# Kernel optimization log

Hardware: AMD Instinct MI355X
Metric: run time of the kernel (lower is better)

The kernel has to match this reference:

```python
import jax, jax.numpy as jnp
import numpy as np

N = 100000       # num nodes
E = 3200000      # num edges (avg degree 32)
F_IN = 128       # num_node_features
HID = 16         # hidden dim hard-coded in Net
C = 10           # num_classes


def setup_inputs() -> dict:
    key = jax.random.key(0)
    k1, k2, k3, k4 = jax.random.split(key, 4)
    x = jax.random.normal(k1, (N, F_IN), dtype=jnp.float32)
    edge_index = jax.random.randint(k2, (2, E), 0, N, dtype=jnp.int32)
    W1 = jax.random.normal(k3, (F_IN, HID), dtype=jnp.float32) * 0.05
    b1 = jnp.zeros((HID,), dtype=jnp.float32)
    W2 = jax.random.normal(k4, (HID, C), dtype=jnp.float32) * 0.05
    b2 = jnp.zeros((C,), dtype=jnp.float32)
    return {"x": x, "edge_index": edge_index, "W1": W1, "b1": b1, "W2": W2, "b2": b2}


def reference(x, edge_index, W1, b1, W2, b2):
    # GCNConv: out = D^{-1/2} (A + I) D^{-1/2} X W + b   (add self-loops)
    loops = jnp.arange(N, dtype=edge_index.dtype)
    row = jnp.concatenate([edge_index[0], loops])  # source nodes
    col = jnp.concatenate([edge_index[1], loops])  # target nodes

    # symmetric normalization (degrees include self-loops, so deg >= 1)
    deg = jax.ops.segment_sum(jnp.ones_like(col, dtype=jnp.float32), col, num_segments=N)
    dis = jax.lax.rsqrt(deg)
    norm = dis[row] * dis[col]  # [E+N]

    def gcn_conv(h, W, b):
        h = h @ W                               # [N, d_out] small GEMM first
        msg = h[row] * norm[:, None]            # gather + scale, [E+N, d_out]
        out = jax.ops.segment_sum(msg, col, num_segments=N)  # scatter-add
        return out + b

    h = jax.nn.relu(gcn_conv(x, W1, b1))
    # F.dropout(training=False) is identity in eval mode
    logits = gcn_conv(h, W2, b2)
    return jax.nn.log_softmax(logits, axis=1)
```

## Files before the change

### kernel.cpp

```cpp
#include <hip/hip_runtime.h>
#include <math.h>

#define N_NODES 100000
#define N_EDGES 3200000
#define F_IN 128
#define HID 16
#define C_OUT 10
#define WIN 128
#define NDIG 782
#define PNB2 512
#define EPB 6250
#define SB1 1564
#define MAXE 28

typedef unsigned short u16;
typedef unsigned int u32;

__device__ __forceinline__ float bf2f(u16 u) {
    return __uint_as_float(((u32)u) << 16);
}
__device__ __forceinline__ u16 f2bf(float f) {
    u32 x = __float_as_uint(f);
    u32 r = (x + 0x7fffu + ((x >> 16) & 1u)) >> 16;
    return (u16)r;
}

__global__ void k_pcnt(const int* __restrict__ col, int* __restrict__ blkhist) {
    __shared__ int h[NDIG];
    for (int i = threadIdx.x; i < NDIG; i += 256) h[i] = 0;
    __syncthreads();
    int lo = blockIdx.x * EPB, hi = lo + EPB;
    for (int e = lo + threadIdx.x; e < hi; e += 256)
        atomicAdd(&h[col[e] >> 7], 1);
    __syncthreads();
    for (int d = threadIdx.x; d < NDIG; d += 256)
        blkhist[d * PNB2 + blockIdx.x] = h[d];
}

__global__ void k_s1(const int* __restrict__ blkhist, int* __restrict__ psum) {
    __shared__ int sm[256];
    int i = blockIdx.x * 256 + threadIdx.x;
    sm[threadIdx.x] = blkhist[i];
    __syncthreads();
    for (int off = 128; off > 0; off >>= 1) {
        if (threadIdx.x < off) sm[threadIdx.x] += sm[threadIdx.x + off];
        __syncthreads();
    }
    if (threadIdx.x == 0) psum[blockIdx.x] = sm[0];
}

__global__ void k_s2(int* __restrict__ psum) {
    const int T = 1024;
    __shared__ int part[T];
    int t = threadIdx.x;
    int i0 = 2 * t, i1 = 2 * t + 1;
    int v0 = (i0 < SB1) ? psum[i0] : 0;
    int v1 = (i1 < SB1) ? psum[i1] : 0;
    part[t] = v0 + v1;
    __syncthreads();
    for (int off = 1; off < T; off <<= 1) {
        int v = part[t];
        int u = (t >= off) ? part[t - off] : 0;
        __syncthreads();
        part[t] = v + u;
        __syncthreads();
    }
    int run = (t > 0) ? part[t - 1] : 0;
    if (i0 < SB1) psum[i0] = run;
    if (i1 < SB1) psum[i1] = run + v0;
}

__global__ void k_s3(int* __restrict__ blkhist, const int* __restrict__ psum) {
    __shared__ int sm[256];
    int i = blockIdx.x * 256 + threadIdx.x;
    int t = threadIdx.x;
    int v = blkhist[i];
    sm[t] = v;
    __syncthreads();
    for (int off = 1; off < 256; off <<= 1) {
        int a = sm[t];
        int b = (t >= off) ? sm[t - off] : 0;
        __syncthreads();
        sm[t] = a + b;
        __syncthreads();
    }
    blkhist[i] = psum[blockIdx.x] + sm[t] - v;
}

__global__ void k_pwrite(const int* __restrict__ row, const int* __restrict__ col,
                         const int* __restrict__ blkhist, u32* __restrict__ staging) {
    __shared__ int base[NDIG];
    __shared__ int lcur[NDIG];
    for (int i = threadIdx.x; i < NDIG; i += 256) {
        base[i] = blkhist[i * PNB2 + blockIdx.x];
        lcur[i] = 0;
    }
    __syncthreads();
    int lo = blockIdx.x * EPB, hi = lo + EPB;
    for (int e = lo + threadIdx.x; e < hi; e += 256) {
        int c = col[e];
        int d = c >> 7;
        int rank = atomicAdd(&lcur[d], 1);
        staging[base[d] + rank] = ((u32)(c & 127) << 17) | (u32)row[e];
    }
}

__global__ void k_csr(u32* staging, const int* __restrict__ blkhist,
                      int* __restrict__ offs, float* __restrict__ dis) {
    __shared__ int cnt[WIN];
    __shared__ int base[WIN];
    int w = blockIdx.x;
    if (threadIdx.x < WIN) cnt[threadIdx.x] = 0;
    __syncthreads();
    int start = blkhist[w * PNB2];
    int end = (w == NDIG - 1) ? N_EDGES : blkhist[(w + 1) * PNB2];
    u32 buf[MAXE];
    int n = 0;
#pragma unroll
    for (int k = 0; k < MAXE; k++) {
        int i = start + k * 256 + (int)threadIdx.x;
        if (i < end) {
            u32 e = staging[i];
            buf[k] = e;
            n = k + 1;
            atomicAdd(&cnt[e >> 17], 1);
        }
    }
    __syncthreads();
    if (threadIdx.x < WIN) base[threadIdx.x] = cnt[threadIdx.x];
    __syncthreads();
    for (int off = 1; off < WIN; off <<= 1) {
        int v = 0;
        if (threadIdx.x < WIN) {
            v = base[threadIdx.x];
            if ((int)threadIdx.x >= off) v += base[threadIdx.x - off];
        }
        __syncthreads();
        if (threadIdx.x < WIN) base[threadIdx.x] = v;
        __syncthreads();
    }
    if (threadIdx.x < WIN) {
        int excl = base[threadIdx.x] - cnt[threadIdx.x];
        base[threadIdx.x] = excl;
        int node = w * WIN + (int)threadIdx.x;
        if (node < N_NODES) {
            offs[node] = start + excl;
            dis[node] = rsqrtf(1.0f + (float)cnt[threadIdx.x]);
        }
    }
    if (w == 0 && threadIdx.x == 0) offs[N_NODES] = N_EDGES;
    __syncthreads();
    if (threadIdx.x < WIN) cnt[threadIdx.x] = 0;
    __syncthreads();
#pragma unroll
    for (int k = 0; k < MAXE; k++) {
        if (k < n) {
            u32 e = buf[k];
            int cl = (int)(e >> 17);
            int rank = atomicAdd(&cnt[cl], 1);
            staging[start + base[cl] + rank] = e;
        }
    }
}

__global__ void k_gemm1(const float* __restrict__ x, const float* __restrict__ W1,
                        const float* __restrict__ dis, u16* __restrict__ h1s) {
    __shared__ float Ws[F_IN * HID];
    for (int t = threadIdx.x; t < F_IN * HID; t += blockDim.x) Ws[t] = W1[t];
    __syncthreads();

    int node = blockIdx.x * blockDim.x + threadIdx.x;
    if (node >= N_NODES) return;

    float acc[HID];
#pragma unroll
    for (int j = 0; j < HID; j++) acc[j] = 0.f;

    const float4* xr = (const float4*)(x + (size_t)node * F_IN);
#pragma unroll 2
    for (int k4 = 0; k4 < F_IN / 4; k4++) {
        float4 v = xr[k4];
        float xv[4] = {v.x, v.y, v.z, v.w};
#pragma unroll
        for (int kk = 0; kk < 4; kk++) {
            const float4* wr = (const float4*)(Ws + (k4 * 4 + kk) * HID);
            float4 w0 = wr[0], w1 = wr[1], w2 = wr[2], w3 = wr[3];
            float xs = xv[kk];
            acc[0]  += xs * w0.x; acc[1]  += xs * w0.y; acc[2]  += xs * w0.z; acc[3]  += xs * w0.w;
            acc[4]  += xs * w1.x; acc[5]  += xs * w1.y; acc[6]  += xs * w1.z; acc[7]  += xs * w1.w;
            acc[8]  += xs * w2.x; acc[9]  += xs * w2.y; acc[10] += xs * w2.z; acc[11] += xs * w2.w;
            acc[12] += xs * w3.x; acc[13] += xs * w3.y; acc[14] += xs * w3.z; acc[15] += xs * w3.w;
        }
    }

    float d = dis[node];
    u32 p[8];
#pragma unroll
    for (int i = 0; i < 8; i++)
        p[i] = (u32)f2bf(acc[2 * i] * d) | ((u32)f2bf(acc[2 * i + 1] * d) << 16);
    u32* dst = (u32*)(h1s + (size_t)node * HID);
#pragma unroll
    for (int i = 0; i < 8; i++) dst[i] = p[i];
}

__global__ void k_gather1(const int* __restrict__ offs, const u32* __restrict__ csr,
                          const float* __restrict__ dis, const u16* __restrict__ h1s,
                          u16* __restrict__ agg1) {
    int t = blockIdx.x * 256 + threadIdx.x;
    int node = t >> 3;
    int f2 = t & 7;
    const u32* hb = (const u32*)h1s;
    u32 v = hb[(size_t)node * 8 + f2];
    float a0 = bf2f((u16)(v & 0xffff));
    float a1 = bf2f((u16)(v >> 16));
    int s0 = offs[node], s1 = offs[node + 1];
    int j = s0;
    for (; j < s1 && (j & 3); j++) {
        int s = (int)(csr[j] & 0x1FFFFu);
        u32 w = hb[(size_t)s * 8 + f2];
        a0 += bf2f((u16)(w & 0xffff));
        a1 += bf2f((u16)(w >> 16));
    }
    for (; j + 4 <= s1; j += 4) {
        uint4 ss = *(const uint4*)(csr + j);
        u32 w0 = hb[(size_t)(ss.x & 0x1FFFFu) * 8 + f2];
        u32 w1 = hb[(size_t)(ss.y & 0x1FFFFu) * 8 + f2];
        u32 w2 = hb[(size_t)(ss.z & 0x1FFFFu) * 8 + f2];
        u32 w3 = hb[(size_t)(ss.w & 0x1FFFFu) * 8 + f2];
        a0 += bf2f((u16)(w0 & 0xffff)); a1 += bf2f((u16)(w0 >> 16));
        a0 += bf2f((u16)(w1 & 0xffff)); a1 += bf2f((u16)(w1 >> 16));
        a0 += bf2f((u16)(w2 & 0xffff)); a1 += bf2f((u16)(w2 >> 16));
        a0 += bf2f((u16)(w3 & 0xffff)); a1 += bf2f((u16)(w3 >> 16));
    }
    for (; j < s1; j++) {
        int s = (int)(csr[j] & 0x1FFFFu);
        u32 w = hb[(size_t)s * 8 + f2];
        a0 += bf2f((u16)(w & 0xffff));
        a1 += bf2f((u16)(w >> 16));
    }
    float dc = dis[node];
    ((u32*)agg1)[(size_t)node * 8 + f2] =
        (u32)f2bf(a0 * dc) | ((u32)f2bf(a1 * dc) << 16);
}

__global__ void k_layer2(const u16* __restrict__ agg1, const float* __restrict__ b1,
                         const float* __restrict__ W2, const float* __restrict__ dis,
                         u16* __restrict__ h2s) {
    __shared__ float Ws[HID * C_OUT];
    __shared__ float b1s[HID];
    if (threadIdx.x < HID * C_OUT) Ws[threadIdx.x] = W2[threadIdx.x];
    if (threadIdx.x < HID) b1s[threadIdx.x] = b1[threadIdx.x];
    __syncthreads();

    int node = blockIdx.x * blockDim.x + threadIdx.x;
    if (node >= N_NODES) return;

    const uint4* ar = (const uint4*)(agg1 + (size_t)node * HID);
    uint4 q0 = ar[0], q1 = ar[1];
    u32 qs[8] = {q0.x, q0.y, q0.z, q0.w, q1.x, q1.y, q1.z, q1.w};

    float acc[C_OUT];
#pragma unroll
    for (int k = 0; k < C_OUT; k++) acc[k] = 0.f;

#pragma unroll
    for (int i = 0; i < 8; i++) {
        u32 q = qs[i];
        float v0 = bf2f((u16)(q & 0xffff));
        float v1 = bf2f((u16)(q >> 16));
        int j0 = 2 * i, j1 = 2 * i + 1;
        float h0 = fmaxf(v0 + b1s[j0], 0.f);
        float h1v = fmaxf(v1 + b1s[j1], 0.f);
#pragma unroll
        for (int k = 0; k < C_OUT; k++) acc[k] += h0 * Ws[j0 * C_OUT + k] + h1v * Ws[j1 * C_OUT + k];
    }

    float d = dis[node];
    u32 p[8];
#pragma unroll
    for (int i = 0; i < 5; i++)
        p[i] = (u32)f2bf(acc[2 * i] * d) | ((u32)f2bf(acc[2 * i + 1] * d) << 16);
    p[5] = 0; p[6] = 0; p[7] = 0;
    u32* dst = (u32*)(h2s + (size_t)node * HID);
#pragma unroll
    for (int i = 0; i < 8; i++) dst[i] = p[i];
}

__global__ void k_gather2(const int* __restrict__ offs, const u32* __restrict__ csr,
                          const float* __restrict__ dis, const u16* __restrict__ h2s,
                          float* __restrict__ agg2) {
    int t = blockIdx.x * 256 + threadIdx.x;
    int node = t >> 3;
    int f2 = t & 7;
    if (f2 >= 5) return;
    const u32* hb = (const u32*)h2s;
    u32 v = hb[(size_t)node * 8 + f2];
    float a0 = bf2f((u16)(v & 0xffff));
    float a1 = bf2f((u16)(v >> 16));
    int s0 = offs[node], s1 = offs[node + 1];
    int j = s0;
    for (; j < s1 && (j & 3); j++) {
        int s = (int)(csr[j] & 0x1FFFFu);
        u32 w = hb[(size_t)s * 8 + f2];
        a0 += bf2f((u16)(w & 0xffff));
        a1 += bf2f((u16)(w >> 16));
    }
    for (; j + 4 <= s1; j += 4) {
        uint4 ss = *(const uint4*)(csr + j);
        u32 w0 = hb[(size_t)(ss.x & 0x1FFFFu) * 8 + f2];
        u32 w1 = hb[(size_t)(ss.y & 0x1FFFFu) * 8 + f2];
        u32 w2 = hb[(size_t)(ss.z & 0x1FFFFu) * 8 + f2];
        u32 w3 = hb[(size_t)(ss.w & 0x1FFFFu) * 8 + f2];
        a0 += bf2f((u16)(w0 & 0xffff)); a1 += bf2f((u16)(w0 >> 16));
        a0 += bf2f((u16)(w1 & 0xffff)); a1 += bf2f((u16)(w1 >> 16));
        a0 += bf2f((u16)(w2 & 0xffff)); a1 += bf2f((u16)(w2 >> 16));
        a0 += bf2f((u16)(w3 & 0xffff)); a1 += bf2f((u16)(w3 >> 16));
    }
    for (; j < s1; j++) {
        int s = (int)(csr[j] & 0x1FFFFu);
        u32 w = hb[(size_t)s * 8 + f2];
        a0 += bf2f((u16)(w & 0xffff));
        a1 += bf2f((u16)(w >> 16));
    }
    float dc = dis[node];
    float2 o = make_float2(a0 * dc, a1 * dc);
    *(float2*)(agg2 + (size_t)node * C_OUT + 2 * f2) = o;
}

__global__ void k_final(float* __restrict__ agg2, const float* __restrict__ b2) {
    __shared__ float b2s[C_OUT];
    if (threadIdx.x < C_OUT) b2s[threadIdx.x] = b2[threadIdx.x];
    __syncthreads();

    int i = blockIdx.x * blockDim.x + threadIdx.x;
    if (i >= N_NODES) return;

    float* ar = agg2 + (size_t)i * C_OUT;
    float v[C_OUT];
    float m = -1e30f;
#pragma unroll
    for (int k = 0; k < C_OUT; k++) {
        v[k] = ar[k] + b2s[k];
        m = fmaxf(m, v[k]);
    }
    float s = 0.f;
#pragma unroll
    for (int k = 0; k < C_OUT; k++) s += expf(v[k] - m);
    float ls = logf(s) + m;
#pragma unroll
    for (int k = 0; k < C_OUT; k++) ar[k] = v[k] - ls;
}

extern "C" void kernel_launch(void* const* d_in, const int* in_sizes, int n_in,
                              void* d_out, int out_size, void* d_ws, size_t ws_size,
                              hipStream_t stream) {
    const float* x  = (const float*)d_in[0];
    const int*   ei = (const int*)d_in[1];
    const float* W1 = (const float*)d_in[2];
    const float* b1 = (const float*)d_in[3];
    const float* W2 = (const float*)d_in[4];
    const float* b2 = (const float*)d_in[5];
    float* out = (float*)d_out;

    const int* row = ei;
    const int* col = ei + N_EDGES;

    char* ws = (char*)d_ws;
    float* dis     = (float*)(ws);
    int*   offs    = (int*)(ws + 400000);
    int*   blkhist = (int*)(ws + 800016);
    int*   psum    = (int*)(ws + 2401552);
    u32*   staging = (u32*)(ws + 2407808);
    u16*   h1s     = (u16*)(ws + 15207808);
    u16*   h2s     = (u16*)(ws + 15207808);
    u16*   agg1    = (u16*)d_out;
    float* agg2    = out;

    const int B = 256;
    int gN  = (N_NODES + B - 1) / B;
    int gN8 = (N_NODES * 8) / B;

    k_pcnt  <<<PNB2, B, 0, stream>>>(col, blkhist);
    k_s1    <<<SB1, B, 0, stream>>>(blkhist, psum);
    k_s2    <<<1, 1024, 0, stream>>>(psum);
    k_s3    <<<SB1, B, 0, stream>>>(blkhist, psum);
    k_pwrite<<<PNB2, B, 0, stream>>>(row, col, blkhist, staging);
    k_csr   <<<NDIG, B, 0, stream>>>(staging, blkhist, offs, dis);
    k_gemm1 <<<gN, B, 0, stream>>>(x, W1, dis, h1s);
    k_gather1<<<gN8, B, 0, stream>>>(offs, staging, dis, h1s, agg1);
    k_layer2<<<gN, B, 0, stream>>>(agg1, b1, W2, dis, h2s);
    k_gather2<<<gN8, B, 0, stream>>>(offs, staging, dis, h2s, agg2);
    k_final <<<gN, B, 0, stream>>>(agg2, b2);
}
```

Before: 260.9 us.

## Widen radix bucket window and stage block-local sort in LDS before scatter

The coarse radix partition moves from 128-node to 256-node windows, which halves the number of buckets and the size of the prefix-scan arrays. k_pwrite now runs 512 threads per block: it first sorts its edges by bucket into shared memory using a local exclusive scan, then writes them out in bucket order. Consecutive threads therefore store to contiguous global addresses instead of scattered ones. A separate copy of the per-block histogram is kept so the local offsets stay available. The costs are extra shared-memory traffic and barriers in k_pwrite, and more registers per thread in k_csr (MAXE goes to 40), which may lower occupancy.

```diff
diff --git a/kernel.cpp b/kernel.cpp
--- a/kernel.cpp
+++ b/kernel.cpp
@@ -6,12 +6,13 @@
 #define F_IN 128
 #define HID 16
 #define C_OUT 10
-#define WIN 128
-#define NDIG 782
+#define WIN 256
+#define NDIG 391
 #define PNB2 512
 #define EPB 6250
-#define SB1 1564
-#define MAXE 28
+#define SCN (NDIG * PNB2)
+#define SB1 782
+#define MAXE 40
 
 typedef unsigned short u16;
 typedef unsigned int u32;
@@ -25,22 +26,22 @@
     return (u16)r;
 }
 
-__global__ void k_pcnt(const int* __restrict__ col, int* __restrict__ blkhist) {
+__global__ void k_pcnt(const int* __restrict__ col, int* __restrict__ blkhistA) {
     __shared__ int h[NDIG];
     for (int i = threadIdx.x; i < NDIG; i += 256) h[i] = 0;
     __syncthreads();
     int lo = blockIdx.x * EPB, hi = lo + EPB;
     for (int e = lo + threadIdx.x; e < hi; e += 256)
-        atomicAdd(&h[col[e] >> 7], 1);
+        atomicAdd(&h[col[e] >> 8], 1);
     __syncthreads();
     for (int d = threadIdx.x; d < NDIG; d += 256)
-        blkhist[d * PNB2 + blockIdx.x] = h[d];
-}
-
-__global__ void k_s1(const int* __restrict__ blkhist, int* __restrict__ psum) {
+        blkhistA[d * PNB2 + blockIdx.x] = h[d];
+}
+
+__global__ void k_s1(const int* __restrict__ blkhistA, int* __restrict__ psum) {
     __shared__ int sm[256];
     int i = blockIdx.x * 256 + threadIdx.x;
-    sm[threadIdx.x] = blkhist[i];
+    sm[threadIdx.x] = blkhistA[i];
     __syncthreads();
     for (int off = 128; off > 0; off >>= 1) {
         if (threadIdx.x < off) sm[threadIdx.x] += sm[threadIdx.x + off];
@@ -53,10 +54,8 @@
     const int T = 1024;
     __shared__ int part[T];
     int t = threadIdx.x;
-    int i0 = 2 * t, i1 = 2 * t + 1;
-    int v0 = (i0 < SB1) ? psum[i0] : 0;
-    int v1 = (i1 < SB1) ? psum[i1] : 0;
-    part[t] = v0 + v1;
+    int v0 = (t < SB1) ? psum[t] : 0;
+    part[t] = v0;
     __syncthreads();
     for (int off = 1; off < T; off <<= 1) {
         int v = part[t];
@@ -65,16 +64,15 @@
         part[t] = v + u;
         __syncthreads();
     }
-    int run = (t > 0) ? part[t - 1] : 0;
-    if (i0 < SB1) psum[i0] = run;
-    if (i1 < SB1) psum[i1] = run + v0;
-}
-
-__global__ void k_s3(int* __restrict__ blkhist, const int* __restrict__ psum) {
+    if (t < SB1) psum[t] = part[t] - v0;
+}
+
+__global__ void k_s3(const int* __restrict__ blkhistA, const int* __restrict__ psum,
+                     int* __restrict__ blkhistB) {
     __shared__ int sm[256];
     int i = blockIdx.x * 256 + threadIdx.x;
     int t = threadIdx.x;
-    int v = blkhist[i];
+    int v = blkhistA[i];
     sm[t] = v;
     __syncthreads();
     for (int off = 1; off < 256; off <<= 1) {
@@ -84,41 +82,71 @@
         sm[t] = a + b;
         __syncthreads();
     }
-    blkhist[i] = psum[blockIdx.x] + sm[t] - v;
+    blkhistB[i] = psum[blockIdx.x] + sm[t] - v;
 }
 
 __global__ void k_pwrite(const int* __restrict__ row, const int* __restrict__ col,
-                         const int* __restrict__ blkhist, u32* __restrict__ staging) {
-    __shared__ int base[NDIG];
+                         const int* __restrict__ blkhistA, const int* __restrict__ blkhistB,
+                         u32* __restrict__ staging) {
+    __shared__ u32 sorted[EPB];
+    __shared__ u16 dwin[EPB];
+    __shared__ int gbase[NDIG];
+    __shared__ int lbase[NDIG];
     __shared__ int lcur[NDIG];
-    for (int i = threadIdx.x; i < NDIG; i += 256) {
-        base[i] = blkhist[i * PNB2 + blockIdx.x];
-        lcur[i] = 0;
-    }
-    __syncthreads();
-    int lo = blockIdx.x * EPB, hi = lo + EPB;
-    for (int e = lo + threadIdx.x; e < hi; e += 256) {
+    __shared__ int scan[512];
+
+    int t = threadIdx.x;
+    int b = blockIdx.x;
+    int hv = 0;
+    if (t < NDIG) {
+        hv = blkhistA[t * PNB2 + b];
+        gbase[t] = blkhistB[t * PNB2 + b];
+        lcur[t] = 0;
+    }
+    scan[t] = hv;
+    __syncthreads();
+    for (int off = 1; off < 512; off <<= 1) {
+        int v = scan[t];
+        int u = (t >= off) ? scan[t - off] : 0;
+        __syncthreads();
+        scan[t] = v + u;
+        __syncthreads();
+    }
+    if (t < NDIG) lbase[t] = scan[t] - hv;
+    __syncthreads();
+
+    int lo = b * EPB, hi = lo + EPB;
+    for (int e = lo + t; e < hi; e += 512) {
         int c = col[e];
-        int d = c >> 7;
+        int d = c >> 8;
         int rank = atomicAdd(&lcur[d], 1);
-        staging[base[d] + rank] = ((u32)(c & 127) << 17) | (u32)row[e];
-    }
-}
-
-__global__ void k_csr(u32* staging, const int* __restrict__ blkhist,
+        int pos = lbase[d] + rank;
+        sorted[pos] = ((u32)(c & 255) << 17) | (u32)row[e];
+        dwin[pos] = (u16)d;
+    }
+    __syncthreads();
+
+    for (int i = t; i < EPB; i += 512) {
+        int d = dwin[i];
+        staging[gbase[d] + (i - lbase[d])] = sorted[i];
+    }
+}
+
+__global__ void k_csr(u32* staging, const int* __restrict__ blkhistB,
                       int* __restrict__ offs, float* __restrict__ dis) {
     __shared__ int cnt[WIN];
     __shared__ int base[WIN];
     int w = blockIdx.x;
-    if (threadIdx.x < WIN) cnt[threadIdx.x] = 0;
-    __syncthreads();
-    int start = blkhist[w * PNB2];
-    int end = (w == NDIG - 1) ? N_EDGES : blkhist[(w + 1) * PNB2];
+    int t = threadIdx.x;
+    cnt[t] = 0;
+    __syncthreads();
+    int start = blkhistB[w * PNB2];
+    int end = (w == NDIG - 1) ? N_EDGES : blkhistB[(w + 1) * PNB2];
     u32 buf[MAXE];
     int n = 0;
 #pragma unroll
     for (int k = 0; k < MAXE; k++) {
-        int i = start + k * 256 + (int)threadIdx.x;
+        int i = start + k * 256 + t;
         if (i < end) {
             u32 e = staging[i];
             buf[k] = e;
@@ -127,30 +155,25 @@
         }
     }
     __syncthreads();
-    if (threadIdx.x < WIN) base[threadIdx.x] = cnt[threadIdx.x];
+    base[t] = cnt[t];
     __syncthreads();
     for (int off = 1; off < WIN; off <<= 1) {
-        int v = 0;
-        if (threadIdx.x < WIN) {
-            v = base[threadIdx.x];
-            if ((int)threadIdx.x >= off) v += base[threadIdx.x - off];
-        }
-        __syncthreads();
-        if (threadIdx.x < WIN) base[threadIdx.x] = v;
-        __syncthreads();
-    }
-    if (threadIdx.x < WIN) {
-        int excl = base[threadIdx.x] - cnt[threadIdx.x];
-        base[threadIdx.x] = excl;
-        int node = w * WIN + (int)threadIdx.x;
-        if (node < N_NODES) {
-            offs[node] = start + excl;
-            dis[node] = rsqrtf(1.0f + (float)cnt[threadIdx.x]);
-        }
-    }
-    if (w == 0 && threadIdx.x == 0) offs[N_NODES] = N_EDGES;
-    __syncthreads();
-    if (threadIdx.x < WIN) cnt[threadIdx.x] = 0;
+        int v = base[t];
+        int u = (t >= off) ? base[t - off] : 0;
+        __syncthreads();
+        base[t] = v + u;
+        __syncthreads();
+    }
+    int excl = base[t] - cnt[t];
+    base[t] = excl;
+    int node = w * WIN + t;
+    if (node < N_NODES) {
+        offs[node] = start + excl;
+        dis[node] = rsqrtf(1.0f + (float)cnt[t]);
+    }
+    if (w == 0 && t == 0) offs[N_NODES] = N_EDGES;
+    __syncthreads();
+    cnt[t] = 0;
     __syncthreads();
 #pragma unroll
     for (int k = 0; k < MAXE; k++) {
@@ -366,26 +389,27 @@
     const int* col = ei + N_EDGES;
 
     char* ws = (char*)d_ws;
-    float* dis     = (float*)(ws);
-    int*   offs    = (int*)(ws + 400000);
-    int*   blkhist = (int*)(ws + 800016);
-    int*   psum    = (int*)(ws + 2401552);
-    u32*   staging = (u32*)(ws + 2407808);
-    u16*   h1s     = (u16*)(ws + 15207808);
-    u16*   h2s     = (u16*)(ws + 15207808);
-    u16*   agg1    = (u16*)d_out;
-    float* agg2    = out;
+    float* dis      = (float*)(ws);
+    int*   offs     = (int*)(ws + 400000);
+    int*   blkhistA = (int*)(ws + 800016);
+    int*   blkhistB = (int*)(ws + 1600784);
+    int*   psum     = (int*)(ws + 2401552);
+    u32*   staging  = (u32*)(ws + 2404688);
+    u16*   h1s      = (u16*)(ws + 15204688);
+    u16*   h2s      = (u16*)(ws + 15204688);
+    u16*   agg1     = (u16*)d_out;
+    float* agg2     = out;
 
     const int B = 256;
     int gN  = (N_NODES + B - 1) / B;
     int gN8 = (N_NODES * 8) / B;
 
-    k_pcnt  <<<PNB2, B, 0, stream>>>(col, blkhist);
-    k_s1    <<<SB1, B, 0, stream>>>(blkhist, psum);
+    k_pcnt  <<<PNB2, B, 0, stream>>>(col, blkhistA);
+    k_s1    <<<SB1, B, 0, stream>>>(blkhistA, psum);
     k_s2    <<<1, 1024, 0, stream>>>(psum);
-    k_s3    <<<SB1, B, 0, stream>>>(blkhist, psum);
-    k_pwrite<<<PNB2, B, 0, stream>>>(row, col, blkhist, staging);
-    k_csr   <<<NDIG, B, 0, stream>>>(staging, blkhist, offs, dis);
+    k_s3    <<<SB1, B, 0, stream>>>(blkhistA, psum, blkhistB);
+    k_pwrite<<<PNB2, 512, 0, stream>>>(row, col, blkhistA, blkhistB, staging);
+    k_csr   <<<NDIG, B, 0, stream>>>(staging, blkhistB, offs, dis);
     k_gemm1 <<<gN, B, 0, stream>>>(x, W1, dis, h1s);
     k_gather1<<<gN8, B, 0, stream>>>(offs, staging, dis, h1s, agg1);
     k_layer2<<<gN, B, 0, stream>>>(agg1, b1, W2, dis, h2s);
```

New measurement: 251.3 us. 1.04x faster.
